# Kernel tuning notes

Measured on AMD Instinct MI355X. Metric: run time of the kernel, lower is better.

The kernel has to match this reference:

```python
import jax, jax.numpy as jnp
import numpy as np
from jax.scipy.linalg import expm

DELTA = 0.01  # time step from __init__ delta
B_SZ, U_DIM, DU_DIM, H_DIM, Y_DIM = 512, 1024, 512, 2048, 1024


def setup_inputs() -> dict:
    key = jax.random.key(0)
    ks = jax.random.split(key, 6)
    inv_sqrt = lambda fan_in: 1.0 / np.sqrt(fan_in)
    u = jax.random.normal(ks[0], (B_SZ, U_DIM), jnp.float32)
    du = jax.random.normal(ks[1], (B_SZ, DU_DIM), jnp.float32)
    # torch.nn.Linear default init: U(-1/sqrt(fan_in), 1/sqrt(fan_in))
    W = jax.random.uniform(ks[2], (H_DIM, H_DIM), jnp.float32, -inv_sqrt(H_DIM), inv_sqrt(H_DIM))
    Bw = jax.random.uniform(ks[3], (H_DIM, U_DIM + DU_DIM), jnp.float32, -inv_sqrt(U_DIM + DU_DIM), inv_sqrt(U_DIM + DU_DIM))
    Cw = jax.random.uniform(ks[4], (Y_DIM, H_DIM), jnp.float32, -inv_sqrt(H_DIM), inv_sqrt(H_DIM))
    h = jax.random.normal(ks[5], (1, H_DIM), jnp.float32)
    return {"u": u, "du": du, "W": W, "Bw": Bw, "Cw": Cw, "h": h}


def reference(u, du, W, Bw, Cw, h):
    # Antisymmetric part of W
    A = 0.5 * (W - W.T)                                    # (H,H)
    A_expm = expm(A * DELTA)                               # (H,H) matrix exponential
    rec = h @ A_expm.T                                     # (1,H) recurrent term: F.linear(h, A_expm)
    A_inv = jnp.linalg.inv(A)                              # (H,H)
    # B(cat([du, u])) : (B, H)
    b = jnp.concatenate([du, u], axis=1) @ Bw.T
    # M = A^{-1} (expm(A*delta) - I); input term = M @ b^T per sample -> b @ M^T
    M = A_inv @ (A_expm - jnp.eye(H_DIM, dtype=A.dtype))   # (H,H)
    inp = b @ M.T                                          # (B,H)
    h_new = rec + inp                                      # broadcast (1,H)+(B,H) -> (B,H)
    y = h_new @ Cw.T                                       # (B,Y)
    return y
```

## Files before the change

### kernel.cpp

```cpp
#include <hip/hip_runtime.h>
#include <hip/hip_bf16.h>


#define B_SZ 512
#define U_DIM 1024
#define DU_DIM 512
#define H_DIM 2048
#define Y_DIM 1024
#define K_CAT 1536
#define DELTA_F 0.01f

typedef __hip_bfloat16 bf16;
using bf16x8f = __attribute__((ext_vector_type(8))) short;
using f32x4   = __attribute__((ext_vector_type(4))) float;

__device__ __forceinline__ short f2bs(float x) {
  union { bf16 b; short s; } u; u.b = __float2bfloat16(x); return u.s;
}
__device__ __forceinline__ int4 pack8(const float4 v0, const float4 v1) {
  union { short s[8]; int4 i; } o;
  o.s[0] = f2bs(v0.x); o.s[1] = f2bs(v0.y); o.s[2] = f2bs(v0.z); o.s[3] = f2bs(v0.w);
  o.s[4] = f2bs(v1.x); o.s[5] = f2bs(v1.y); o.s[6] = f2bs(v1.z); o.s[7] = f2bs(v1.w);
  return o.i;
}

__device__ __forceinline__ void stage16(const void* g, void* l) {
  __builtin_amdgcn_global_load_lds(
      (const __attribute__((address_space(1))) unsigned int*)g,
      (__attribute__((address_space(3))) unsigned int*)l, 16, 0, 0);
}

#define NB   (H_DIM * K_CAT / 8)
#define NCAT (B_SZ * K_CAT / 8)
#define NC   (Y_DIM * H_DIM / 8)
#define NTOT (NB + NCAT + NC)

__global__ __launch_bounds__(256) void k1(const float* __restrict__ W, const float* __restrict__ h,
                                          const float* __restrict__ Bw, const float* __restrict__ du,
                                          const float* __restrict__ u, const float* __restrict__ Cw,
                                          float* __restrict__ wh, float* __restrict__ wtp,
                                          short* __restrict__ Bwb, short* __restrict__ catb,
                                          short* __restrict__ Cwb) {
  const int b = blockIdx.x;
  if (b < 512) {
    const int lane = threadIdx.x & 63, wave = threadIdx.x >> 6;
    const int row = b * 4 + wave;
    const float* wr = W + (size_t)row * H_DIM;
    float s = 0.f;
#pragma unroll
    for (int it = 0; it < 8; it++) {
      int k = it * 256 + lane * 4;
      float4 a = *(const float4*)(wr + k);
      float4 hv = *(const float4*)(h + k);
      s += a.x * hv.x + a.y * hv.y + a.z * hv.z + a.w * hv.w;
    }
#pragma unroll
    for (int off = 32; off > 0; off >>= 1) s += __shfl_down(s, off);
    if (lane == 0) wh[row] = s;
  } else if (b < 768) {
    const int e = b - 512;
    const int colg = e & 7, rowg = e >> 3;
    const int k = colg * 256 + threadIdx.x;
    float s = 0.f;
    const float* base = W + (size_t)rowg * 64 * H_DIM + k;
#pragma unroll 8
    for (int i = 0; i < 64; i++) s += base[(size_t)i * H_DIM] * h[rowg * 64 + i];
    wtp[rowg * H_DIM + k] = s;
  } else {
    for (int g = (b - 768) * 256 + threadIdx.x; g < NTOT; g += 256 * 256) {
      if (g < NB) {
        int e = g * 8;
        *(int4*)(Bwb + e) = pack8(*(const float4*)(Bw + e), *(const float4*)(Bw + e + 4));
      } else if (g < NB + NCAT) {
        int g2 = g - NB;
        int row = g2 / 192, c = g2 - row * 192;
        const float* src = (c < 64) ? du + (size_t)row * DU_DIM + c * 8
                                    : u + (size_t)row * U_DIM + (c - 64) * 8;
        *(int4*)(catb + (size_t)row * K_CAT + c * 8) =
            pack8(*(const float4*)src, *(const float4*)(src + 4));
      } else {
        int e = (g - NB - NCAT) * 8;
        *(int4*)(Cwb + e) = pack8(*(const float4*)(Cw + e), *(const float4*)(Cw + e + 4));
      }
    }
  }
}

#define MFMA __builtin_amdgcn_mfma_f32_16x16x32_bf16

__global__ __launch_bounds__(256) void k2(const short* __restrict__ catb, const short* __restrict__ Bwb,
                                          const float* __restrict__ h, const float* __restrict__ wh,
                                          const float* __restrict__ wtp, short* __restrict__ bb) {
  __shared__ __align__(16) short lds[2 * 6144];
  __shared__ float recf[64];
  const int tid = threadIdx.x;
  const int lane = tid & 63, wave = tid >> 6;
  const int wm = wave >> 1, wn = wave & 1;
  const int mt = blockIdx.x >> 5, nt = blockIdx.x & 31;
  const int row0 = mt * 32, col0 = nt * 64;
  const int rA = tid >> 3, gA = tid & 7;
  const int sA = (gA ^ (rA & 7)) * 8;
  const short* srcA  = catb + (size_t)(row0 + rA) * K_CAT + sA;
  const short* srcB1 = Bwb + (size_t)(col0 + rA) * K_CAT + sA;
  const short* srcB2 = Bwb + (size_t)(col0 + 32 + rA) * K_CAT + sA;
  const int NT = K_CAT / 64;
  const int rm = lane & 15, quad = lane >> 4;
  f32x4 acc[2] = {};
  stage16(srcA,  lds + tid * 8);
  stage16(srcB1, lds + 2048 + tid * 8);
  stage16(srcB2, lds + 4096 + tid * 8);
  __syncthreads();
  const int ra = wm * 16 + rm;
  const int rb0 = wn * 32 + rm, rb1 = wn * 32 + 16 + rm;
  const int oa = ra * 64, ob0 = rb0 * 64, ob1 = rb1 * 64;
  const int xa = (ra & 7), xb0 = (rb0 & 7), xb1 = (rb1 & 7);
  for (int kt = 0; kt < NT; kt++) {
    const int cur = kt & 1;
    if (kt + 1 < NT) {
      const int o = (kt + 1) * 64;
      short* nb = lds + (cur ^ 1) * 6144;
      stage16(srcA + o,  nb + tid * 8);
      stage16(srcB1 + o, nb + 2048 + tid * 8);
      stage16(srcB2 + o, nb + 4096 + tid * 8);
    }
    const short* Ac = lds + cur * 6144;
    const short* Bc = Ac + 2048;
#pragma unroll
    for (int ks = 0; ks < 2; ks++) {
      const int kg = ks * 4 + quad;
      bf16x8f af  = *(const bf16x8f*)&Ac[oa + ((kg ^ xa) << 3)];
      bf16x8f bf0 = *(const bf16x8f*)&Bc[ob0 + ((kg ^ xb0) << 3)];
      bf16x8f bf1 = *(const bf16x8f*)&Bc[ob1 + ((kg ^ xb1) << 3)];
      acc[0] = MFMA(af, bf0, acc[0], 0, 0, 0);
      acc[1] = MFMA(af, bf1, acc[1], 0, 0, 0);
    }
    if (kt + 1 < NT) __syncthreads();
  }
  if (tid < 64) {
    int gc = col0 + tid;
    float s = 0.f;
#pragma unroll
    for (int p = 0; p < 32; p++) s += wtp[p * H_DIM + gc];
    recf[tid] = h[gc] + 0.005f * (wh[gc] - s);
  }
  __syncthreads();
#pragma unroll
  for (int j = 0; j < 2; j++) {
    int gc = col0 + wn * 32 + 16 * j + rm;
#pragma unroll
    for (int r = 0; r < 4; r++) {
      int gr = row0 + wm * 16 + quad * 4 + r;
      bb[(size_t)gr * H_DIM + gc] = f2bs(recf[gc - col0] + DELTA_F * acc[j][r]);
    }
  }
}

__global__ __launch_bounds__(256) void k3(const short* __restrict__ A, const short* __restrict__ B,
                                          float* __restrict__ y) {
  __shared__ __align__(16) short lds[2 * 4096];
  const int tid = threadIdx.x;
  const int lane = tid & 63, wave = tid >> 6;
  const int wm = wave >> 1, wn = wave & 1;
  const int mt = blockIdx.x >> 5, nt = blockIdx.x & 31;
  const int row0 = mt * 32, col0 = nt * 32;
  const int rA = tid >> 3, gA = tid & 7;
  const int sA = (gA ^ (rA & 7)) * 8;
  const short* srcA = A + (size_t)(row0 + rA) * H_DIM + sA;
  const short* srcB = B + (size_t)(col0 + rA) * H_DIM + sA;
  const int NT = H_DIM / 64;
  const int rm = lane & 15, quad = lane >> 4;
  f32x4 acc = {};
  stage16(srcA, lds + tid * 8);
  stage16(srcB, lds + 2048 + tid * 8);
  __syncthreads();
  const int ra = wm * 16 + rm, rb = wn * 16 + rm;
  const int oa = ra * 64, ob = rb * 64;
  const int xa = (ra & 7), xb = (rb & 7);
  for (int kt = 0; kt < NT; kt++) {
    const int cur = kt & 1;
    if (kt + 1 < NT) {
      const int o = (kt + 1) * 64;
      short* nb = lds + (cur ^ 1) * 4096;
      stage16(srcA + o, nb + tid * 8);
      stage16(srcB + o, nb + 2048 + tid * 8);
    }
    const short* Ac = lds + cur * 4096;
    const short* Bc = Ac + 2048;
#pragma unroll
    for (int ks = 0; ks < 2; ks++) {
      const int kg = ks * 4 + quad;
      bf16x8f af = *(const bf16x8f*)&Ac[oa + ((kg ^ xa) << 3)];
      bf16x8f bf = *(const bf16x8f*)&Bc[ob + ((kg ^ xb) << 3)];
      acc = MFMA(af, bf, acc, 0, 0, 0);
    }
    if (kt + 1 < NT) __syncthreads();
  }
  int gc = col0 + wn * 16 + rm;
#pragma unroll
  for (int r = 0; r < 4; r++) {
    int gr = row0 + wm * 16 + quad * 4 + r;
    y[(size_t)gr * Y_DIM + gc] = acc[r];
  }
}

extern "C" void kernel_launch(void* const* d_in, const int* in_sizes, int n_in,
                              void* d_out, int out_size, void* d_ws, size_t ws_size,
                              hipStream_t stream) {
  const float* u  = (const float*)d_in[0];
  const float* du = (const float*)d_in[1];
  const float* W  = (const float*)d_in[2];
  const float* Bw = (const float*)d_in[3];
  const float* Cw = (const float*)d_in[4];
  const float* h  = (const float*)d_in[5];
  float* y = (float*)d_out;

  char* w = (char*)d_ws;
  size_t off = 0;
  short* Bwb  = (short*)(w + off); off += (size_t)H_DIM * K_CAT * sizeof(short);
  short* Cwb  = (short*)(w + off); off += (size_t)Y_DIM * H_DIM * sizeof(short);
  short* bb   = (short*)(w + off); off += (size_t)B_SZ * H_DIM * sizeof(short);
  short* catb = (short*)(w + off); off += (size_t)B_SZ * K_CAT * sizeof(short);
  float* wh   = (float*)(w + off); off += H_DIM * sizeof(float);
  float* wtp  = (float*)(w + off); off += 32 * H_DIM * sizeof(float);
  if (ws_size < off) return;

  k1<<<1024, 256, 0, stream>>>(W, h, Bw, du, u, Cw, wh, wtp, Bwb, catb, Cwb);
  k2<<<1024, 256, 0, stream>>>(catb, Bwb, h, wh, wtp, bb);
  k3<<<512, 256, 0, stream>>>(bb, Cwb, y);
}
```

Baseline: 128.7 us.

## Fuse W·h and Wᵀ·h into one pass; move Cw conversion into GEMM kernel

The row dot products W·h and column dot products Wᵀ·h are now computed in a single pass over W. Each block reads a 64x256 tile once, producing per-column partials and per-row partials reduced through wave shuffles and shared memory. This halves the reads of the 16 MB W matrix. The Cw-to-bf16 conversion moves out of k1 into spare blocks of k2, which frees k1 blocks for the Bw/cat conversion and overlaps the Cw work with the first GEMM. The cost is a shuffle reduction per row inside the loop and an extra partial-sum read in k2's epilogue.

New measurement: 157.2 us. +22.2%, slower.

```diff
diff --git a/kernel.cpp b/kernel.cpp
--- a/kernel.cpp
+++ b/kernel.cpp
@@ -33,54 +33,50 @@
 #define NB   (H_DIM * K_CAT / 8)
 #define NCAT (B_SZ * K_CAT / 8)
 #define NC   (Y_DIM * H_DIM / 8)
-#define NTOT (NB + NCAT + NC)
 
 __global__ __launch_bounds__(256) void k1(const float* __restrict__ W, const float* __restrict__ h,
                                           const float* __restrict__ Bw, const float* __restrict__ du,
-                                          const float* __restrict__ u, const float* __restrict__ Cw,
-                                          float* __restrict__ wh, float* __restrict__ wtp,
-                                          short* __restrict__ Bwb, short* __restrict__ catb,
-                                          short* __restrict__ Cwb) {
+                                          const float* __restrict__ u, float* __restrict__ whp,
+                                          float* __restrict__ wtp, short* __restrict__ Bwb,
+                                          short* __restrict__ catb) {
   const int b = blockIdx.x;
-  if (b < 512) {
+  if (b < 256) {
+    const int rowg = b >> 3, colg = b & 7;
+    const int r0 = rowg * 64;
+    const int k = colg * 256 + threadIdx.x;
     const int lane = threadIdx.x & 63, wave = threadIdx.x >> 6;
-    const int row = b * 4 + wave;
-    const float* wr = W + (size_t)row * H_DIM;
-    float s = 0.f;
-#pragma unroll
-    for (int it = 0; it < 8; it++) {
-      int k = it * 256 + lane * 4;
-      float4 a = *(const float4*)(wr + k);
-      float4 hv = *(const float4*)(h + k);
-      s += a.x * hv.x + a.y * hv.y + a.z * hv.z + a.w * hv.w;
-    }
-#pragma unroll
-    for (int off = 32; off > 0; off >>= 1) s += __shfl_down(s, off);
-    if (lane == 0) wh[row] = s;
-  } else if (b < 768) {
-    const int e = b - 512;
-    const int colg = e & 7, rowg = e >> 3;
-    const int k = colg * 256 + threadIdx.x;
-    float s = 0.f;
-    const float* base = W + (size_t)rowg * 64 * H_DIM + k;
+    __shared__ float rowred[64][4];
+    const float* base = W + (size_t)r0 * H_DIM + k;
+    const float hk = h[k];
+    float scol = 0.f;
 #pragma unroll 8
-    for (int i = 0; i < 64; i++) s += base[(size_t)i * H_DIM] * h[rowg * 64 + i];
-    wtp[rowg * H_DIM + k] = s;
+    for (int i = 0; i < 64; i++) {
+      float v = base[(size_t)i * H_DIM];
+      scol += v * h[r0 + i];
+      float p = v * hk;
+#pragma unroll
+      for (int off = 32; off > 0; off >>= 1) p += __shfl_down(p, off);
+      if (lane == 0) rowred[i][wave] = p;
+    }
+    wtp[rowg * H_DIM + k] = scol;
+    __syncthreads();
+    if (threadIdx.x < 64) {
+      float s = rowred[threadIdx.x][0] + rowred[threadIdx.x][1] +
+                rowred[threadIdx.x][2] + rowred[threadIdx.x][3];
+      whp[colg * H_DIM + r0 + threadIdx.x] = s;
+    }
   } else {
-    for (int g = (b - 768) * 256 + threadIdx.x; g < NTOT; g += 256 * 256) {
+    for (int g = (b - 256) * 256 + threadIdx.x; g < NB + NCAT; g += 768 * 256) {
       if (g < NB) {
         int e = g * 8;
         *(int4*)(Bwb + e) = pack8(*(const float4*)(Bw + e), *(const float4*)(Bw + e + 4));
-      } else if (g < NB + NCAT) {
+      } else {
         int g2 = g - NB;
         int row = g2 / 192, c = g2 - row * 192;
         const float* src = (c < 64) ? du + (size_t)row * DU_DIM + c * 8
                                     : u + (size_t)row * U_DIM + (c - 64) * 8;
         *(int4*)(catb + (size_t)row * K_CAT + c * 8) =
             pack8(*(const float4*)src, *(const float4*)(src + 4));
-      } else {
-        int e = (g - NB - NCAT) * 8;
-        *(int4*)(Cwb + e) = pack8(*(const float4*)(Cw + e), *(const float4*)(Cw + e + 4));
       }
     }
   }
@@ -89,14 +85,24 @@
 #define MFMA __builtin_amdgcn_mfma_f32_16x16x32_bf16
 
 __global__ __launch_bounds__(256) void k2(const short* __restrict__ catb, const short* __restrict__ Bwb,
-                                          const float* __restrict__ h, const float* __restrict__ wh,
-                                          const float* __restrict__ wtp, short* __restrict__ bb) {
+                                          const float* __restrict__ h, const float* __restrict__ whp,
+                                          const float* __restrict__ wtp, short* __restrict__ bb,
+                                          const float* __restrict__ Cw, short* __restrict__ Cwb) {
   __shared__ __align__(16) short lds[2 * 6144];
   __shared__ float recf[64];
+  const int b = blockIdx.x;
+  if (b >= 512) {
+    int g0 = (b - 512) * 256 + threadIdx.x;
+    int e = g0 * 8;
+    *(int4*)(Cwb + e) = pack8(*(const float4*)(Cw + e), *(const float4*)(Cw + e + 4));
+    e = (g0 + 131072) * 8;
+    *(int4*)(Cwb + e) = pack8(*(const float4*)(Cw + e), *(const float4*)(Cw + e + 4));
+    return;
+  }
   const int tid = threadIdx.x;
   const int lane = tid & 63, wave = tid >> 6;
   const int wm = wave >> 1, wn = wave & 1;
-  const int mt = blockIdx.x >> 5, nt = blockIdx.x & 31;
+  const int mt = b >> 5, nt = b & 31;
   const int row0 = mt * 32, col0 = nt * 64;
   const int rA = tid >> 3, gA = tid & 7;
   const int sA = (gA ^ (rA & 7)) * 8;
@@ -138,10 +144,12 @@
   }
   if (tid < 64) {
     int gc = col0 + tid;
-    float s = 0.f;
-#pragma unroll
-    for (int p = 0; p < 32; p++) s += wtp[p * H_DIM + gc];
-    recf[tid] = h[gc] + 0.005f * (wh[gc] - s);
+    float sw = 0.f, st = 0.f;
+#pragma unroll
+    for (int g = 0; g < 8; g++) sw += whp[g * H_DIM + gc];
+#pragma unroll
+    for (int p = 0; p < 32; p++) st += wtp[p * H_DIM + gc];
+    recf[tid] = h[gc] + 0.005f * (sw - st);
   }
   __syncthreads();
 #pragma unroll
@@ -220,11 +228,11 @@
   short* Cwb  = (short*)(w + off); off += (size_t)Y_DIM * H_DIM * sizeof(short);
   short* bb   = (short*)(w + off); off += (size_t)B_SZ * H_DIM * sizeof(short);
   short* catb = (short*)(w + off); off += (size_t)B_SZ * K_CAT * sizeof(short);
-  float* wh   = (float*)(w + off); off += H_DIM * sizeof(float);
+  float* whp  = (float*)(w + off); off += 8 * H_DIM * sizeof(float);
   float* wtp  = (float*)(w + off); off += 32 * H_DIM * sizeof(float);
   if (ws_size < off) return;
 
-  k1<<<1024, 256, 0, stream>>>(W, h, Bw, du, u, Cw, wh, wtp, Bwb, catb, Cwb);
-  k2<<<1024, 256, 0, stream>>>(catb, Bwb, h, wh, wtp, bb);
+  k1<<<1024, 256, 0, stream>>>(W, h, Bw, du, u, whp, wtp, Bwb, catb);
+  k2<<<1024, 256, 0, stream>>>(catb, Bwb, h, whp, wtp, bb, Cw, Cwb);
   k3<<<512, 256, 0, stream>>>(bb, Cwb, y);
 }
```
